# Performance work log

Measured on AMD Instinct MI355X. Metric: run time of the kernel, lower is better.

The kernel has to match this reference:

```python
import jax, jax.numpy as jnp
import numpy as np

NEG_INF = -9e15  # matches torch's -9000000000000000.0 mask value


def setup_inputs() -> dict:
    key = jax.random.key(0)
    k1, k2, k3, k4 = jax.random.split(key, 4)
    B, F_in, T, N, F_out = 8, 64, 12, 512, 64
    inp = {
        "input": jax.random.normal(k1, (B, F_in, T, N), dtype=jnp.float32),
        "adj": jax.random.randint(k2, (B, T, N, N), 0, 2, dtype=jnp.int32),
        "W": jax.random.normal(k3, (F_in, F_out), dtype=jnp.float32),
        "a": jax.random.normal(k4, (2 * F_out, 1), dtype=jnp.float32),
    }
    return inp


def reference(input, adj, W, a):
    # input: [B, F_in, T, N], adj: [B, T, N, N]
    F_out = W.shape[1]
    x = jnp.transpose(input, (0, 2, 3, 1))          # [B, T, N, F_in]
    Wh = jnp.einsum('btnf,fo->btno', x, W)          # [B, T, N, F_out]
    # score decomposition: e[i,j] = leakyrelu(a1.Wh_i + a2.Wh_j)
    a1 = a[:F_out, 0]
    a2 = a[F_out:, 0]
    f1 = Wh @ a1                                    # [B, T, N]
    f2 = Wh @ a2                                    # [B, T, N]
    e = jax.nn.leaky_relu(f1[..., :, None] + f2[..., None, :], 0.2)
    e = jnp.where(adj > 0, e, NEG_INF)
    attn = jax.nn.softmax(e, axis=-1)               # [B, T, N, N]
    h = jnp.einsum('btij,btjo->btio', attn, Wh)     # [B, T, N, F_out]
    return jax.nn.elu(h)                            # concat=True -> elu
```

## Files before the change

### kernel.cpp

```cpp
#include <hip/hip_runtime.h>
#include <hip/hip_bf16.h>

typedef float fx4 __attribute__((ext_vector_type(4)));
typedef short i16x8 __attribute__((ext_vector_type(8)));
typedef unsigned short u16;

#define NEG_INF_F (-9.0e15f)

__device__ inline u16 f2bf(float v){
  __hip_bfloat16 h = __float2bfloat16(v);
  return *reinterpret_cast<u16*>(&h);
}

__global__ __launch_bounds__(256) void gat_prep(
    const float* __restrict__ input,
    const float* __restrict__ W,
    const float* __restrict__ Avec,
    u16*   __restrict__ whT,
    float* __restrict__ f1w,
    float* __restrict__ f2w)
{
  __shared__ float Wl[64*64];
  __shared__ float Al[128];
  const int tid = threadIdx.x;
  const int bt  = blockIdx.y;
  const int b   = bt / 12, t = bt % 12;
  const int n   = blockIdx.x * 256 + tid;

  {
    const fx4* src = (const fx4*)W;
    fx4* dst = (fx4*)Wl;
    #pragma unroll
    for (int i = 0; i < 4; ++i) dst[tid + 256*i] = src[tid + 256*i];
    if (tid < 32) ((fx4*)Al)[tid] = ((const fx4*)Avec)[tid];
  }
  __syncthreads();

  const float* xp = input + ((size_t)b*64*12 + t) * 512 + n;

  fx4 acc[16];
  #pragma unroll
  for (int i = 0; i < 16; ++i) acc[i] = (fx4){0.f,0.f,0.f,0.f};

  #pragma unroll 8
  for (int f = 0; f < 64; ++f) {
    float xv = xp[(size_t)f * 6144];
    const fx4* wr = (const fx4*)(Wl + f*64);
    #pragma unroll
    for (int o4 = 0; o4 < 16; ++o4) acc[o4] += xv * wr[o4];
  }

  float s1 = 0.f, s2 = 0.f;
  #pragma unroll
  for (int o4 = 0; o4 < 16; ++o4) {
    fx4 v  = acc[o4];
    fx4 w1 = ((const fx4*)Al)[o4];
    fx4 w2 = ((const fx4*)Al)[o4 + 16];
    s1 += v[0]*w1[0] + v[1]*w1[1] + v[2]*w1[2] + v[3]*w1[3];
    s2 += v[0]*w2[0] + v[1]*w2[1] + v[2]*w2[2] + v[3]*w2[3];
  }
  f1w[bt*512 + n] = s1;
  f2w[bt*512 + n] = s2;

  u16* wp = whT + (size_t)bt*64*512 + n;
  #pragma unroll
  for (int o4 = 0; o4 < 16; ++o4) {
    #pragma unroll
    for (int c = 0; c < 4; ++c)
      wp[(size_t)(o4*4 + c) * 512] = f2bf(acc[o4][c]);
  }
}

__global__ __launch_bounds__(256) void gat_attn(
    const int*   __restrict__ adj,
    const u16*   __restrict__ whT,
    const float* __restrict__ f1w,
    const float* __restrict__ f2w,
    float*       __restrict__ out)
{
  __shared__ float f2l[512];
  __shared__ float f1l[16];
  __shared__ float sums[16];
  __shared__ u16   attnl[16*512];

  const int tid = threadIdx.x;
  const int l   = tid & 63;
  const int w   = tid >> 6;
  const int bt  = blockIdx.y;
  const int it  = blockIdx.x;

  ((float2*)f2l)[tid] = ((const float2*)(f2w + bt*512))[tid];
  if (tid < 16) f1l[tid] = f1w[bt*512 + it*16 + tid];
  __syncthreads();

  const int R0     = w * 4;
  const int row_g0 = it*16 + R0;
  const int4* adj4 = (const int4*)(adj + (size_t)bt*512*512);

  int4 pre[4][2];
  #pragma unroll
  for (int p = 0; p < 4; ++p) {
    const int4* ar = adj4 + (size_t)(row_g0 + p) * 128;
    pre[p][0] = ar[l];
    pre[p][1] = ar[64 + l];
  }

  const fx4 f20 = ((const fx4*)f2l)[l];
  const fx4 f21 = ((const fx4*)f2l)[64 + l];

  float psum[4];
  #pragma unroll
  for (int r = 0; r < 4; ++r) {
    const int4 c0 = pre[r][0];
    const int4 c1 = pre[r][1];
    const float f1v = f1l[R0 + r];

    float e[8], m = NEG_INF_F;
#define GAT_E(idx, cc, ff) { float s = f1v + (ff); float lr = s > 0.f ? s : 0.2f*s; \
                             e[idx] = ((cc) > 0) ? lr : NEG_INF_F; m = fmaxf(m, e[idx]); }
    GAT_E(0, c0.x, f20[0]) GAT_E(1, c0.y, f20[1]) GAT_E(2, c0.z, f20[2]) GAT_E(3, c0.w, f20[3])
    GAT_E(4, c1.x, f21[0]) GAT_E(5, c1.y, f21[1]) GAT_E(6, c1.z, f21[2]) GAT_E(7, c1.w, f21[3])
#undef GAT_E
    #pragma unroll
    for (int off = 32; off >= 1; off >>= 1) m = fmaxf(m, __shfl_xor(m, off));

    float p[8], sum = 0.f;
    #pragma unroll
    for (int i = 0; i < 8; ++i) { p[i] = __expf(e[i] - m); sum += p[i]; }
    psum[r] = sum;

    const int rowR = R0 + r;
    const unsigned swz = (unsigned)((rowR & 7) << 4);
    char* base = (char*)attnl + rowR * 1024;
    ushort4 pk0, pk1;
    pk0.x = f2bf(p[0]); pk0.y = f2bf(p[1]); pk0.z = f2bf(p[2]); pk0.w = f2bf(p[3]);
    pk1.x = f2bf(p[4]); pk1.y = f2bf(p[5]); pk1.z = f2bf(p[6]); pk1.w = f2bf(p[7]);
    *(ushort4*)(base + (((unsigned)(      8*l)) ^ swz)) = pk0;
    *(ushort4*)(base + (((unsigned)(512 + 8*l)) ^ swz)) = pk1;
  }

  #pragma unroll
  for (int r = 0; r < 4; ++r) {
    #pragma unroll
    for (int off = 32; off >= 1; off >>= 1) psum[r] += __shfl_xor(psum[r], off);
  }
  if (l == 0) {
    #pragma unroll
    for (int r = 0; r < 4; ++r) sums[R0 + r] = psum[r];
  }

  __syncthreads();

  const int r = l & 15, q = l >> 4;
  const unsigned swzB = (unsigned)((r & 7) << 4);
  const char* aBase = (const char*)attnl + r * 1024;
  const u16*  wb    = whT + (size_t)bt*64*512 + (size_t)(w*16 + r)*512;
  fx4 acc = {0,0,0,0};

  #pragma unroll
  for (int jt = 0; jt < 512; jt += 32) {
    i16x8 af = *(const i16x8*)(aBase + (((unsigned)(jt*2 + q*16)) ^ swzB));
    i16x8 bf = *(const i16x8*)(wb + jt + 8*q);
    acc = __builtin_amdgcn_mfma_f32_16x16x32_bf16(af, bf, acc, 0, 0, 0);
  }

  float* op = out + ((size_t)bt*512 + it*16) * 64;
  #pragma unroll
  for (int rr = 0; rr < 4; ++rr) {
    const float rs = 1.0f / sums[q*4 + rr];
    float v = acc[rr] * rs;
    v = v > 0.f ? v : expm1f(v);
    op[(q*4 + rr)*64 + w*16 + r] = v;
  }
}

extern "C" void kernel_launch(void* const* d_in, const int* in_sizes, int n_in,
                              void* d_out, int out_size, void* d_ws, size_t ws_size,
                              hipStream_t stream) {
  const float* input = (const float*)d_in[0];
  const int*   adj   = (const int*)  d_in[1];
  const float* W     = (const float*)d_in[2];
  const float* Avec  = (const float*)d_in[3];
  float* out = (float*)d_out;

  char* ws = (char*)d_ws;
  u16*   whT = (u16*)ws;
  float* f1w = (float*)(ws + 6291456);
  float* f2w = (float*)(ws + 6291456 + 196608);

  gat_prep<<<dim3(2, 96), 256, 0, stream>>>(input, W, Avec, whT, f1w, f2w);
  gat_attn<<<dim3(32, 96), 256, 0, stream>>>(adj, whT, f1w, f2w, out);
}
```

Baseline: 62.29 us.

## Factor softmax exponentials, pre-pack Wh into MFMA fragment layout, pipeline adj loads

The softmax exponent is factored into per-column terms exp(f2-F2max) and exp(0.2*(f2-F2max)), computed once per block, times per-row scalars. This removes per-element transcendentals, with a fallback exact path when the row's masked-max gap is large. The prep kernel now writes Wh in a blocked layout staged through shared memory, so the MFMA B-operand load becomes one contiguous 16-byte read per lane. Adjacency row loads are double-buffered to cut register pressure, and launch bounds request 4 blocks per CU; the factored form risks precision loss if the gap test misjudges underflow.

```diff
diff --git a/kernel.cpp b/kernel.cpp
--- a/kernel.cpp
+++ b/kernel.cpp
@@ -16,16 +16,18 @@
     const float* __restrict__ input,
     const float* __restrict__ W,
     const float* __restrict__ Avec,
-    u16*   __restrict__ whT,
+    u16*   __restrict__ whB,
     float* __restrict__ f1w,
     float* __restrict__ f2w)
 {
   __shared__ float Wl[64*64];
   __shared__ float Al[128];
+  __shared__ u16   Rp[16384];
   const int tid = threadIdx.x;
   const int bt  = blockIdx.y;
   const int b   = bt / 12, t = bt % 12;
-  const int n   = blockIdx.x * 256 + tid;
+  const int xb  = blockIdx.x;
+  const int n   = xb * 256 + tid;
 
   {
     const fx4* src = (const fx4*)W;
@@ -62,24 +64,36 @@
   f1w[bt*512 + n] = s1;
   f2w[bt*512 + n] = s2;
 
-  u16* wp = whT + (size_t)bt*64*512 + n;
+  const int ktl  = (n >> 5) & 7;
+  const int q    = (n >> 3) & 3;
+  const int e    = n & 7;
+  const int rowb = ktl*2048 + q*128 + e;
   #pragma unroll
   for (int o4 = 0; o4 < 16; ++o4) {
     #pragma unroll
-    for (int c = 0; c < 4; ++c)
-      wp[(size_t)(o4*4 + c) * 512] = f2bf(acc[o4][c]);
-  }
-}
-
-__global__ __launch_bounds__(256) void gat_attn(
+    for (int c = 0; c < 4; ++c) {
+      const int o = o4*4 + c;
+      Rp[rowb + (o >> 4)*512 + (o & 15)*8] = f2bf(acc[o4][c]);
+    }
+  }
+  __syncthreads();
+
+  uint4* dst = (uint4*)(whB + ((size_t)bt*16 + xb*8) * 2048);
+  const uint4* src = (const uint4*)Rp;
+  #pragma unroll
+  for (int i = 0; i < 8; ++i) dst[tid + 256*i] = src[tid + 256*i];
+}
+
+__global__ __launch_bounds__(256, 4) void gat_attn(
     const int*   __restrict__ adj,
-    const u16*   __restrict__ whT,
+    const u16*   __restrict__ whB,
     const float* __restrict__ f1w,
     const float* __restrict__ f2w,
     float*       __restrict__ out)
 {
   __shared__ float f2l[512];
   __shared__ float f1l[16];
+  __shared__ float wmax[4];
   __shared__ float sums[16];
   __shared__ u16   attnl[16*512];
 
@@ -89,52 +103,105 @@
   const int bt  = blockIdx.y;
   const int it  = blockIdx.x;
 
-  ((float2*)f2l)[tid] = ((const float2*)(f2w + bt*512))[tid];
+  float2 fv = ((const float2*)(f2w + bt*512))[tid];
+  ((float2*)f2l)[tid] = fv;
+  float m2 = fmaxf(fv.x, fv.y);
+  #pragma unroll
+  for (int off = 32; off >= 1; off >>= 1) m2 = fmaxf(m2, __shfl_xor(m2, off));
+  if (l == 0) wmax[w] = m2;
   if (tid < 16) f1l[tid] = f1w[bt*512 + it*16 + tid];
   __syncthreads();
+  const float F2max = fmaxf(fmaxf(wmax[0], wmax[1]), fmaxf(wmax[2], wmax[3]));
+
+  const fx4 f20 = ((const fx4*)f2l)[l];
+  const fx4 f21 = ((const fx4*)f2l)[64 + l];
+  fx4 v0, v1, vh0, vh1;
+  #pragma unroll
+  for (int c = 0; c < 4; ++c) {
+    v0[c]  = __expf(f20[c] - F2max);
+    v1[c]  = __expf(f21[c] - F2max);
+    vh0[c] = __expf(0.2f*(f20[c] - F2max));
+    vh1[c] = __expf(0.2f*(f21[c] - F2max));
+  }
 
   const int R0     = w * 4;
   const int row_g0 = it*16 + R0;
   const int4* adj4 = (const int4*)(adj + (size_t)bt*512*512);
 
-  int4 pre[4][2];
-  #pragma unroll
-  for (int p = 0; p < 4; ++p) {
+  int4 pre[2][2];
+  #pragma unroll
+  for (int p = 0; p < 2; ++p) {
     const int4* ar = adj4 + (size_t)(row_g0 + p) * 128;
     pre[p][0] = ar[l];
     pre[p][1] = ar[64 + l];
   }
 
-  const fx4 f20 = ((const fx4*)f2l)[l];
-  const fx4 f21 = ((const fx4*)f2l)[64 + l];
-
-  float psum[4];
+  float ssum[4];
   #pragma unroll
   for (int r = 0; r < 4; ++r) {
-    const int4 c0 = pre[r][0];
-    const int4 c1 = pre[r][1];
+    const int4 c0 = pre[r & 1][0];
+    const int4 c1 = pre[r & 1][1];
+    if (r + 2 < 4) {
+      const int4* ar = adj4 + (size_t)(row_g0 + r + 2) * 128;
+      pre[r & 1][0] = ar[l];
+      pre[r & 1][1] = ar[64 + l];
+    }
     const float f1v = f1l[R0 + r];
 
-    float e[8], m = NEG_INF_F;
-#define GAT_E(idx, cc, ff) { float s = f1v + (ff); float lr = s > 0.f ? s : 0.2f*s; \
-                             e[idx] = ((cc) > 0) ? lr : NEG_INF_F; m = fmaxf(m, e[idx]); }
-    GAT_E(0, c0.x, f20[0]) GAT_E(1, c0.y, f20[1]) GAT_E(2, c0.z, f20[2]) GAT_E(3, c0.w, f20[3])
-    GAT_E(4, c1.x, f21[0]) GAT_E(5, c1.y, f21[1]) GAT_E(6, c1.z, f21[2]) GAT_E(7, c1.w, f21[3])
-#undef GAT_E
-    #pragma unroll
-    for (int off = 32; off >= 1; off >>= 1) m = fmaxf(m, __shfl_xor(m, off));
-
-    float p[8], sum = 0.f;
-    #pragma unroll
-    for (int i = 0; i < 8; ++i) { p[i] = __expf(e[i] - m); sum += p[i]; }
-    psum[r] = sum;
+    float mx = NEG_INF_F;
+    mx = fmaxf(mx, (c0.x > 0) ? f20[0] : NEG_INF_F);
+    mx = fmaxf(mx, (c0.y > 0) ? f20[1] : NEG_INF_F);
+    mx = fmaxf(mx, (c0.z > 0) ? f20[2] : NEG_INF_F);
+    mx = fmaxf(mx, (c0.w > 0) ? f20[3] : NEG_INF_F);
+    mx = fmaxf(mx, (c1.x > 0) ? f21[0] : NEG_INF_F);
+    mx = fmaxf(mx, (c1.y > 0) ? f21[1] : NEG_INF_F);
+    mx = fmaxf(mx, (c1.z > 0) ? f21[2] : NEG_INF_F);
+    mx = fmaxf(mx, (c1.w > 0) ? f21[3] : NEG_INF_F);
+    #pragma unroll
+    for (int off = 32; off >= 1; off >>= 1) mx = fmaxf(mx, __shfl_xor(mx, off));
+
+    const float tM = f1v + mx;
+    const float M  = fmaxf(tM, 0.2f*tM);
+    const float gap = F2max - mx;
+
+    float sum = 0.f;
+    ushort4 pk0, pk1;
+    if (gap <= 80.f) {
+      const float u  = __expf(f1v + F2max - M);
+      const float uh = __expf(0.2f*(f1v + F2max) - M);
+      const float thr = -f1v;
+      float pv;
+#define GAT_F(pkf, cc, ff, vv, vvh) { \
+      const bool cpos = (ff) > thr; \
+      float a = cpos ? (vv) : (vvh); \
+      float bb = cpos ? u : uh; \
+      pv = ((cc) > 0) ? a*bb : 0.f; sum += pv; pkf = f2bf(pv); }
+      GAT_F(pk0.x, c0.x, f20[0], v0[0], vh0[0])
+      GAT_F(pk0.y, c0.y, f20[1], v0[1], vh0[1])
+      GAT_F(pk0.z, c0.z, f20[2], v0[2], vh0[2])
+      GAT_F(pk0.w, c0.w, f20[3], v0[3], vh0[3])
+      GAT_F(pk1.x, c1.x, f21[0], v1[0], vh1[0])
+      GAT_F(pk1.y, c1.y, f21[1], v1[1], vh1[1])
+      GAT_F(pk1.z, c1.z, f21[2], v1[2], vh1[2])
+      GAT_F(pk1.w, c1.w, f21[3], v1[3], vh1[3])
+#undef GAT_F
+    } else {
+      const float Mf = (mx == NEG_INF_F) ? NEG_INF_F : M;
+      float pv;
+#define GAT_S(pkf, cc, ff) { float s = f1v + (ff); float lr = fmaxf(s, 0.2f*s); \
+      float ee = ((cc) > 0) ? lr : NEG_INF_F; \
+      pv = __expf(ee - Mf); sum += pv; pkf = f2bf(pv); }
+      GAT_S(pk0.x, c0.x, f20[0]) GAT_S(pk0.y, c0.y, f20[1])
+      GAT_S(pk0.z, c0.z, f20[2]) GAT_S(pk0.w, c0.w, f20[3])
+      GAT_S(pk1.x, c1.x, f21[0]) GAT_S(pk1.y, c1.y, f21[1])
+      GAT_S(pk1.z, c1.z, f21[2]) GAT_S(pk1.w, c1.w, f21[3])
+#undef GAT_S
+    }
+    ssum[r] = sum;
 
     const int rowR = R0 + r;
     const unsigned swz = (unsigned)((rowR & 7) << 4);
     char* base = (char*)attnl + rowR * 1024;
-    ushort4 pk0, pk1;
-    pk0.x = f2bf(p[0]); pk0.y = f2bf(p[1]); pk0.z = f2bf(p[2]); pk0.w = f2bf(p[3]);
-    pk1.x = f2bf(p[4]); pk1.y = f2bf(p[5]); pk1.z = f2bf(p[6]); pk1.w = f2bf(p[7]);
     *(ushort4*)(base + (((unsigned)(      8*l)) ^ swz)) = pk0;
     *(ushort4*)(base + (((unsigned)(512 + 8*l)) ^ swz)) = pk1;
   }
@@ -142,25 +209,25 @@
   #pragma unroll
   for (int r = 0; r < 4; ++r) {
     #pragma unroll
-    for (int off = 32; off >= 1; off >>= 1) psum[r] += __shfl_xor(psum[r], off);
+    for (int off = 32; off >= 1; off >>= 1) ssum[r] += __shfl_xor(ssum[r], off);
   }
   if (l == 0) {
     #pragma unroll
-    for (int r = 0; r < 4; ++r) sums[R0 + r] = psum[r];
-  }
-
+    for (int r = 0; r < 4; ++r) sums[R0 + r] = ssum[r];
+  }
   __syncthreads();
 
   const int r = l & 15, q = l >> 4;
+  const int ct = w;
   const unsigned swzB = (unsigned)((r & 7) << 4);
   const char* aBase = (const char*)attnl + r * 1024;
-  const u16*  wb    = whT + (size_t)bt*64*512 + (size_t)(w*16 + r)*512;
+  const u16*  wp    = whB + (size_t)bt*32768 + ct*512 + l*8;
   fx4 acc = {0,0,0,0};
 
   #pragma unroll
-  for (int jt = 0; jt < 512; jt += 32) {
-    i16x8 af = *(const i16x8*)(aBase + (((unsigned)(jt*2 + q*16)) ^ swzB));
-    i16x8 bf = *(const i16x8*)(wb + jt + 8*q);
+  for (int kt = 0; kt < 16; ++kt) {
+    i16x8 af = *(const i16x8*)(aBase + (((unsigned)(kt*64 + q*16)) ^ swzB));
+    i16x8 bf = *(const i16x8*)(wp + kt*2048);
     acc = __builtin_amdgcn_mfma_f32_16x16x32_bf16(af, bf, acc, 0, 0, 0);
   }
 
@@ -170,7 +237,7 @@
     const float rs = 1.0f / sums[q*4 + rr];
     float v = acc[rr] * rs;
     v = v > 0.f ? v : expm1f(v);
-    op[(q*4 + rr)*64 + w*16 + r] = v;
+    op[(q*4 + rr)*64 + ct*16 + r] = v;
   }
 }
 
@@ -184,10 +251,10 @@
   float* out = (float*)d_out;
 
   char* ws = (char*)d_ws;
-  u16*   whT = (u16*)ws;
+  u16*   whB = (u16*)ws;
   float* f1w = (float*)(ws + 6291456);
   float* f2w = (float*)(ws + 6291456 + 196608);
 
-  gat_prep<<<dim3(2, 96), 256, 0, stream>>>(input, W, Avec, whT, f1w, f2w);
-  gat_attn<<<dim3(32, 96), 256, 0, stream>>>(adj, whT, f1w, f2w, out);
-}
+  gat_prep<<<dim3(2, 96), 256, 0, stream>>>(input, W, Avec, whB, f1w, f2w);
+  gat_attn<<<dim3(32, 96), 256, 0, stream>>>(adj, whB, f1w, f2w, out);
+}
```

Measured after the change: 50.62 us. 18.7% less time.
